# Optimization experiments

Measured on AMD Instinct MI355X. Metric: run time of the kernel, lower is better.

Reference implementation:

```python
import jax, jax.numpy as jnp
import numpy as np


def setup_inputs() -> dict:
    key = jax.random.key(0)
    ks = jax.random.split(key, 8)
    n_src, n_dst, n_edges = 100000, 50000, 600000
    d_in, d_out = 128, 128
    n_reuse, n_cache = 5000, 8000
    full_dst_len = n_dst + n_reuse

    feat_src = jax.random.normal(ks[0], (n_src, d_in), jnp.float32)
    src = jax.random.randint(ks[1], (n_edges,), 0, n_src)
    dst = jax.random.randint(ks[2], (n_edges,), 0, n_dst)
    # xavier-ish init for the two bias-free Linear layers (stored as [out, in] like torch)
    W_self = jax.random.normal(ks[3], (d_out, d_in), jnp.float32) / np.sqrt(d_in).astype(np.float32)
    W_neigh = jax.random.normal(ks[4], (d_out, d_in), jnp.float32) / np.sqrt(d_in).astype(np.float32)
    # reuse_indices must be unique positions within [0, full_dst_len)
    reuse_indices = jnp.sort(jax.random.permutation(ks[5], full_dst_len)[:n_reuse])
    reuse_embedding = jax.random.normal(ks[6], (n_reuse, d_out), jnp.float32)
    cache_indices = jax.random.randint(ks[7], (n_cache,), 0, full_dst_len)
    return dict(feat_src=feat_src, W_self=W_self, W_neigh=W_neigh,
                reuse_embedding=reuse_embedding, src=src, dst=dst,
                reuse_indices=reuse_indices, cache_indices=cache_indices,
                n_dst=n_dst)


def reference(feat_src, W_self, W_neigh, reuse_embedding, src, dst,
              reuse_indices, cache_indices, n_dst):
    # --- GraphSAGE 'mean' aggregation on a block graph ---
    feat_dst = feat_src[:n_dst]                         # [n_dst, D_in]
    msgs = feat_src[src]                                # [E, D_in] copy_src gather
    ssum = jax.ops.segment_sum(msgs, dst, num_segments=n_dst)          # [n_dst, D_in]
    deg = jax.ops.segment_sum(jnp.ones_like(msgs[:, 0]), dst, num_segments=n_dst)
    h_neigh = jnp.where(deg[:, None] > 0, ssum / jnp.maximum(deg, 1.0)[:, None], 0.0)
    rst = feat_dst @ W_self.T + h_neigh @ W_neigh.T     # fc_self + fc_neigh

    # --- cache-reuse scatter merge (flag == 0 path) ---
    n_reuse = reuse_indices.shape[0]
    full_dst_len = n_dst + n_reuse
    keep = jnp.ones((full_dst_len,), dtype=bool).at[reuse_indices].set(False)
    unprune_indices = jnp.nonzero(keep, size=n_dst)[0]  # np.delete equivalent
    full = jnp.zeros((full_dst_len, rst.shape[1]), rst.dtype)
    full = full.at[unprune_indices].set(rst).at[reuse_indices].set(reuse_embedding)
    cache_embedding = jax.lax.stop_gradient(full[cache_indices])  # .detach()
    return full, cache_embedding
```

## Files before the change

kernel.cpp:

```cpp
#include <hip/hip_runtime.h>

#define N_DST   50000
#define D       128
#define MAXDEG  128

typedef __attribute__((ext_vector_type(8))) short bf16x8;
typedef __attribute__((ext_vector_type(4))) float f32x4;

__device__ __forceinline__ unsigned short f2bf(float f) {
    unsigned u = __float_as_uint(f);
    u += 0x7FFFu + ((u >> 16) & 1u);
    return (unsigned short)(u >> 16);
}

__global__ void build_ell_kernel(const int* __restrict__ src,
                                 const int* __restrict__ dst,
                                 int* __restrict__ ell,
                                 int* __restrict__ cnt,
                                 int n_edges) {
    int e = blockIdx.x * blockDim.x + threadIdx.x;
    if (e >= n_edges) return;
    int d = dst[e];
    int pos = atomicAdd(&cnt[d], 1);
    if (pos < MAXDEG)
        ell[(size_t)d * MAXDEG + pos] = src[e];
}

__global__ void rowpos_kernel(const int* __restrict__ reuse_idx,
                              int* __restrict__ rowpos, int n_reuse) {
    int i = blockIdx.x * blockDim.x + threadIdx.x;
    if (i >= N_DST) return;
    int lo = 0, hi = n_reuse;
    while (lo < hi) {
        int mid = (lo + hi) >> 1;
        if (reuse_idx[mid] - mid > i) hi = mid; else lo = mid + 1;
    }
    rowpos[i] = i + lo;
}

__global__ void wconv_kernel(const float* __restrict__ Wself,
                             const float* __restrict__ Wneigh,
                             unsigned short* __restrict__ wbf) {
    int idx = blockIdx.x * blockDim.x + threadIdx.x;
    if (idx >= 128 * 256) return;
    int n = idx >> 8;
    int k = idx & 255;
    float v = (k < 128) ? Wself[n * 128 + k] : Wneigh[n * 128 + (k - 128)];
    wbf[idx] = f2bf(v);
}

__global__ __launch_bounds__(256)
void gather_kernel(const float* __restrict__ feat,
                   const int* __restrict__ ell,
                   const int* __restrict__ cnt,
                   unsigned int* __restrict__ hneigh_u32) {
    int gid  = blockIdx.x * blockDim.x + threadIdx.x;
    int row  = gid >> 6;
    int lane = threadIdx.x & 63;
    if (row >= N_DST) return;

    int deg = cnt[row];
    int n = min(deg, MAXDEG);
    float inv = 1.0f / fmaxf((float)deg, 1.0f);
    const int* rell = ell + (size_t)row * MAXDEG;

    float2 acc = make_float2(0.f, 0.f);
    int j = 0;
    for (; j + 4 <= n; j += 4) {
        int s0 = rell[j + 0];
        int s1 = rell[j + 1];
        int s2 = rell[j + 2];
        int s3 = rell[j + 3];
        float2 v0 = *(const float2*)&feat[(size_t)s0 * D + 2 * lane];
        float2 v1 = *(const float2*)&feat[(size_t)s1 * D + 2 * lane];
        float2 v2 = *(const float2*)&feat[(size_t)s2 * D + 2 * lane];
        float2 v3 = *(const float2*)&feat[(size_t)s3 * D + 2 * lane];
        acc.x += v0.x + v1.x + v2.x + v3.x;
        acc.y += v0.y + v1.y + v2.y + v3.y;
    }
    for (; j < n; ++j) {
        int s = rell[j];
        float2 v = *(const float2*)&feat[(size_t)s * D + 2 * lane];
        acc.x += v.x;
        acc.y += v.y;
    }
    unsigned lo16 = f2bf(acc.x * inv);
    unsigned hi16 = f2bf(acc.y * inv);
    hneigh_u32[(size_t)row * 64 + lane] = lo16 | (hi16 << 16);
}

__global__ __launch_bounds__(256, 2)
void gemm_kernel(const float* __restrict__ feat,
                 const unsigned short* __restrict__ hneigh,
                 const unsigned short* __restrict__ wbf,
                 const int* __restrict__ rowpos,
                 float* __restrict__ full) {
    __shared__ unsigned short Wl[128 * 256];

    int tid = threadIdx.x;
    {
        int n = tid >> 1;
        int ckbase = (tid & 1) * 16;
        const uint4* s = (const uint4*)(wbf + n * 256);
        uint4* d = (uint4*)(Wl + n * 256);
#pragma unroll
        for (int i = 0; i < 16; ++i) {
            int ck = ckbase + i;
            d[ck ^ (n & 7)] = s[ck];
        }
    }
    __syncthreads();

    int wv   = tid >> 6;
    int lane = tid & 63;
    int l15  = lane & 15;
    int q    = lane >> 4;
    int rowbase = blockIdx.x * 128 + wv * 32;

    f32x4 acc[2][8];
#pragma unroll
    for (int rt = 0; rt < 2; ++rt)
#pragma unroll
        for (int ct = 0; ct < 8; ++ct) acc[rt][ct] = (f32x4){0.f, 0.f, 0.f, 0.f};

    int r0c = min(rowbase + l15,      N_DST - 1);
    int r1c = min(rowbase + 16 + l15, N_DST - 1);

#pragma unroll 1
    for (int s = 0; s < 4; ++s) {
        int k0 = s * 32 + q * 8;
        float4 a0lo = *(const float4*)(feat + (size_t)r0c * D + k0);
        float4 a0hi = *(const float4*)(feat + (size_t)r0c * D + k0 + 4);
        float4 a1lo = *(const float4*)(feat + (size_t)r1c * D + k0);
        float4 a1hi = *(const float4*)(feat + (size_t)r1c * D + k0 + 4);
        union { bf16x8 v; unsigned short u[8]; } a0, a1;
        a0.u[0] = f2bf(a0lo.x); a0.u[1] = f2bf(a0lo.y);
        a0.u[2] = f2bf(a0lo.z); a0.u[3] = f2bf(a0lo.w);
        a0.u[4] = f2bf(a0hi.x); a0.u[5] = f2bf(a0hi.y);
        a0.u[6] = f2bf(a0hi.z); a0.u[7] = f2bf(a0hi.w);
        a1.u[0] = f2bf(a1lo.x); a1.u[1] = f2bf(a1lo.y);
        a1.u[2] = f2bf(a1lo.z); a1.u[3] = f2bf(a1lo.w);
        a1.u[4] = f2bf(a1hi.x); a1.u[5] = f2bf(a1hi.y);
        a1.u[6] = f2bf(a1hi.z); a1.u[7] = f2bf(a1hi.w);
#pragma unroll
        for (int ct = 0; ct < 8; ++ct) {
            int n = ct * 16 + l15;
            int ck = s * 4 + q;
            bf16x8 b = *(const bf16x8*)(Wl + n * 256 + ((ck ^ (n & 7)) << 3));
            acc[0][ct] = __builtin_amdgcn_mfma_f32_16x16x32_bf16(a0.v, b, acc[0][ct], 0, 0, 0);
            acc[1][ct] = __builtin_amdgcn_mfma_f32_16x16x32_bf16(a1.v, b, acc[1][ct], 0, 0, 0);
        }
    }
#pragma unroll 1
    for (int s = 0; s < 4; ++s) {
        int k0 = s * 32 + q * 8;
        bf16x8 a0 = *(const bf16x8*)(hneigh + (size_t)r0c * D + k0);
        bf16x8 a1 = *(const bf16x8*)(hneigh + (size_t)r1c * D + k0);
#pragma unroll
        for (int ct = 0; ct < 8; ++ct) {
            int n = ct * 16 + l15;
            int ck = 16 + s * 4 + q;
            bf16x8 b = *(const bf16x8*)(Wl + n * 256 + ((ck ^ (n & 7)) << 3));
            acc[0][ct] = __builtin_amdgcn_mfma_f32_16x16x32_bf16(a0, b, acc[0][ct], 0, 0, 0);
            acc[1][ct] = __builtin_amdgcn_mfma_f32_16x16x32_bf16(a1, b, acc[1][ct], 0, 0, 0);
        }
    }

#pragma unroll
    for (int rt = 0; rt < 2; ++rt) {
#pragma unroll
        for (int reg = 0; reg < 4; ++reg) {
            int gm = rowbase + rt * 16 + q * 4 + reg;
            if (gm < N_DST) {
                int jj = rowpos[gm];
                float* outr = full + (size_t)jj * D + l15;
#pragma unroll
                for (int ct = 0; ct < 8; ++ct)
                    outr[ct * 16] = acc[rt][ct][reg];
            }
        }
    }
}

__global__ void reuse_copy_kernel(const float* __restrict__ emb,
                                  const int* __restrict__ ridx,
                                  float* __restrict__ full, int n) {
    int idx = blockIdx.x * blockDim.x + threadIdx.x;
    int r = idx >> 5;
    if (r >= n) return;
    int c4 = (idx & 31) * 4;
    *(float4*)&full[ridx[r] * D + c4] = *(const float4*)&emb[r * D + c4];
}

__global__ void cache_gather_kernel(const float* __restrict__ full,
                                    const int* __restrict__ cidx,
                                    float* __restrict__ out, int n) {
    int idx = blockIdx.x * blockDim.x + threadIdx.x;
    int r = idx >> 5;
    if (r >= n) return;
    int c4 = (idx & 31) * 4;
    *(float4*)&out[r * D + c4] = *(const float4*)&full[cidx[r] * D + c4];
}

extern "C" void kernel_launch(void* const* d_in, const int* in_sizes, int n_in,
                              void* d_out, int out_size, void* d_ws, size_t ws_size,
                              hipStream_t stream) {
    const float* feat_src  = (const float*)d_in[0];
    const float* W_self    = (const float*)d_in[1];
    const float* W_neigh   = (const float*)d_in[2];
    const float* reuse_emb = (const float*)d_in[3];
    const int*   src       = (const int*)d_in[4];
    const int*   dst       = (const int*)d_in[5];
    const int*   reuse_idx = (const int*)d_in[6];
    const int*   cache_idx = (const int*)d_in[7];

    int n_edges = in_sizes[4];
    int n_reuse = in_sizes[6];
    int n_cache = in_sizes[7];
    int full_len = N_DST + n_reuse;

    unsigned short* hneigh = (unsigned short*)d_ws;
    int*   cnt    = (int*)(hneigh + (size_t)N_DST * D);
    int*   rowpos = cnt + N_DST;
    unsigned short* wbf = (unsigned short*)(rowpos + N_DST);

    float* full = (float*)d_out;
    float* cache_out = full + (size_t)full_len * D;

    int* ell = (int*)full;

    hipMemsetAsync(cnt, 0, (size_t)N_DST * sizeof(int), stream);

    build_ell_kernel<<<(n_edges + 255) / 256, 256, 0, stream>>>(
        src, dst, ell, cnt, n_edges);

    rowpos_kernel<<<(N_DST + 255) / 256, 256, 0, stream>>>(
        reuse_idx, rowpos, n_reuse);

    wconv_kernel<<<(128 * 256 + 255) / 256, 256, 0, stream>>>(
        W_self, W_neigh, wbf);

    gather_kernel<<<(N_DST * 64 + 255) / 256, 256, 0, stream>>>(
        feat_src, ell, cnt, (unsigned int*)hneigh);

    gemm_kernel<<<(N_DST + 127) / 128, 256, 0, stream>>>(
        feat_src, hneigh, wbf, rowpos, full);

    reuse_copy_kernel<<<(n_reuse * 32 + 255) / 256, 256, 0, stream>>>(
        reuse_emb, reuse_idx, full, n_reuse);

    cache_gather_kernel<<<(n_cache * 32 + 255) / 256, 256, 0, stream>>>(
        full, cache_idx, cache_out, n_cache);
}
```

Measured before the change: 204.9 us.

## Fuse neighbor gather with GEMM over a bf16 feature copy, merge prep kernels

```diff
diff --git a/kernel.cpp b/kernel.cpp
--- a/kernel.cpp
+++ b/kernel.cpp
@@ -2,7 +2,8 @@
 
 #define N_DST   50000
 #define D       128
-#define MAXDEG  128
+#define ELLW    64
+#define ELLW_FB 128
 
 typedef __attribute__((ext_vector_type(8))) short bf16x8;
 typedef __attribute__((ext_vector_type(4))) float f32x4;
@@ -12,65 +13,179 @@
     u += 0x7FFFu + ((u >> 16) & 1u);
     return (unsigned short)(u >> 16);
 }
+__device__ __forceinline__ void acc8_add(float* a, uint4 p) {
+    a[0] += __uint_as_float(p.x << 16);
+    a[1] += __uint_as_float(p.x & 0xffff0000u);
+    a[2] += __uint_as_float(p.y << 16);
+    a[3] += __uint_as_float(p.y & 0xffff0000u);
+    a[4] += __uint_as_float(p.z << 16);
+    a[5] += __uint_as_float(p.z & 0xffff0000u);
+    a[6] += __uint_as_float(p.w << 16);
+    a[7] += __uint_as_float(p.w & 0xffff0000u);
+}
 
 __global__ void build_ell_kernel(const int* __restrict__ src,
                                  const int* __restrict__ dst,
                                  int* __restrict__ ell,
                                  int* __restrict__ cnt,
-                                 int n_edges) {
+                                 int n_edges, int width) {
     int e = blockIdx.x * blockDim.x + threadIdx.x;
     if (e >= n_edges) return;
     int d = dst[e];
     int pos = atomicAdd(&cnt[d], 1);
-    if (pos < MAXDEG)
-        ell[(size_t)d * MAXDEG + pos] = src[e];
-}
-
-__global__ void rowpos_kernel(const int* __restrict__ reuse_idx,
-                              int* __restrict__ rowpos, int n_reuse) {
-    int i = blockIdx.x * blockDim.x + threadIdx.x;
-    if (i >= N_DST) return;
-    int lo = 0, hi = n_reuse;
-    while (lo < hi) {
-        int mid = (lo + hi) >> 1;
-        if (reuse_idx[mid] - mid > i) hi = mid; else lo = mid + 1;
-    }
-    rowpos[i] = i + lo;
-}
-
-__global__ void wconv_kernel(const float* __restrict__ Wself,
-                             const float* __restrict__ Wneigh,
-                             unsigned short* __restrict__ wbf) {
+    if (pos < width)
+        ell[(size_t)d * width + pos] = src[e];
+}
+
+__global__ void prep_kernel(const float* __restrict__ feat,
+                            const float* __restrict__ Wself,
+                            const float* __restrict__ Wneigh,
+                            const int* __restrict__ reuse_idx,
+                            unsigned short* __restrict__ featb,
+                            unsigned short* __restrict__ wbf,
+                            int* __restrict__ rowpos,
+                            int n_src16, int n_reuse) {
     int idx = blockIdx.x * blockDim.x + threadIdx.x;
-    if (idx >= 128 * 256) return;
-    int n = idx >> 8;
-    int k = idx & 255;
-    float v = (k < 128) ? Wself[n * 128 + k] : Wneigh[n * 128 + (k - 128)];
-    wbf[idx] = f2bf(v);
+    if (featb != nullptr && idx < n_src16) {
+        const float* s = feat + (size_t)idx * 8;
+        float4 v0 = *(const float4*)s;
+        float4 v1 = *(const float4*)(s + 4);
+        union { unsigned short u[8]; uint4 q; } o;
+        o.u[0] = f2bf(v0.x); o.u[1] = f2bf(v0.y);
+        o.u[2] = f2bf(v0.z); o.u[3] = f2bf(v0.w);
+        o.u[4] = f2bf(v1.x); o.u[5] = f2bf(v1.y);
+        o.u[6] = f2bf(v1.z); o.u[7] = f2bf(v1.w);
+        *(uint4*)(featb + (size_t)idx * 8) = o.q;
+    }
+    if (idx < 128 * 256) {
+        int n = idx >> 8, k = idx & 255;
+        float v = (k < 128) ? Wself[n * 128 + k] : Wneigh[n * 128 + (k - 128)];
+        wbf[idx] = f2bf(v);
+    }
+    if (idx < N_DST) {
+        int lo = 0, hi = n_reuse;
+        while (lo < hi) {
+            int m = (lo + hi) >> 1;
+            if (reuse_idx[m] - m > idx) hi = m; else lo = m + 1;
+        }
+        rowpos[idx] = idx + lo;
+    }
+}
+
+#define HNS 136
+__global__ __launch_bounds__(256, 4)
+void fused_kernel(const unsigned short* __restrict__ featb,
+                  const int* __restrict__ ell,
+                  const int* __restrict__ cnt,
+                  const unsigned short* __restrict__ wbf,
+                  const int* __restrict__ rowpos,
+                  float* __restrict__ full) {
+    __shared__ unsigned short hnl[64 * HNS];
+
+    int tid = threadIdx.x;
+    int r0 = blockIdx.x * 64;
+
+    {
+        int c = tid & 15;
+        int rowslot = tid >> 4;
+#pragma unroll 1
+        for (int i = 0; i < 4; ++i) {
+            int rl = rowslot + 16 * i;
+            int row = r0 + rl;
+            float acc[8] = {0.f, 0.f, 0.f, 0.f, 0.f, 0.f, 0.f, 0.f};
+            if (row < N_DST) {
+                int deg = cnt[row];
+                int n = min(deg, ELLW);
+                const int* rell = ell + (size_t)row * ELLW;
+                int j = 0;
+                for (; j + 4 <= n; j += 4) {
+                    int s0 = rell[j + 0];
+                    int s1 = rell[j + 1];
+                    int s2 = rell[j + 2];
+                    int s3 = rell[j + 3];
+                    uint4 p0 = *(const uint4*)(featb + (size_t)s0 * D + 8 * c);
+                    uint4 p1 = *(const uint4*)(featb + (size_t)s1 * D + 8 * c);
+                    uint4 p2 = *(const uint4*)(featb + (size_t)s2 * D + 8 * c);
+                    uint4 p3 = *(const uint4*)(featb + (size_t)s3 * D + 8 * c);
+                    acc8_add(acc, p0); acc8_add(acc, p1);
+                    acc8_add(acc, p2); acc8_add(acc, p3);
+                }
+                for (; j < n; ++j) {
+                    int s = rell[j];
+                    uint4 p = *(const uint4*)(featb + (size_t)s * D + 8 * c);
+                    acc8_add(acc, p);
+                }
+                float inv = 1.0f / fmaxf((float)deg, 1.0f);
+#pragma unroll
+                for (int k = 0; k < 8; ++k) acc[k] *= inv;
+            }
+            union { unsigned short u[8]; uint4 q; } o;
+#pragma unroll
+            for (int k = 0; k < 8; ++k) o.u[k] = f2bf(acc[k]);
+            *(uint4*)&hnl[rl * HNS + 8 * c] = o.q;
+        }
+    }
+    __syncthreads();
+
+    int wv = tid >> 6, lane = tid & 63;
+    int l15 = lane & 15, q = lane >> 4;
+    int rowbase = r0 + wv * 16;
+
+    f32x4 acc[8];
+#pragma unroll
+    for (int ct = 0; ct < 8; ++ct) acc[ct] = (f32x4){0.f, 0.f, 0.f, 0.f};
+
+    int rA = min(rowbase + l15, N_DST - 1);
+    const unsigned short* aptr = featb + (size_t)rA * D;
+#pragma unroll 1
+    for (int s = 0; s < 4; ++s) {
+        bf16x8 a = *(const bf16x8*)(aptr + s * 32 + q * 8);
+#pragma unroll
+        for (int ct = 0; ct < 8; ++ct) {
+            bf16x8 b = *(const bf16x8*)(wbf + (ct * 16 + l15) * 256 + s * 32 + q * 8);
+            acc[ct] = __builtin_amdgcn_mfma_f32_16x16x32_bf16(a, b, acc[ct], 0, 0, 0);
+        }
+    }
+    const unsigned short* hrow = hnl + (wv * 16 + l15) * HNS;
+#pragma unroll 1
+    for (int s = 0; s < 4; ++s) {
+        bf16x8 a = *(const bf16x8*)(hrow + s * 32 + q * 8);
+#pragma unroll
+        for (int ct = 0; ct < 8; ++ct) {
+            bf16x8 b = *(const bf16x8*)(wbf + (ct * 16 + l15) * 256 + 128 + s * 32 + q * 8);
+            acc[ct] = __builtin_amdgcn_mfma_f32_16x16x32_bf16(a, b, acc[ct], 0, 0, 0);
+        }
+    }
+
+#pragma unroll
+    for (int reg = 0; reg < 4; ++reg) {
+        int gm = rowbase + q * 4 + reg;
+        if (gm < N_DST) {
+            float* outr = full + (size_t)rowpos[gm] * D + l15;
+#pragma unroll
+            for (int ct = 0; ct < 8; ++ct)
+                outr[ct * 16] = acc[ct][reg];
+        }
+    }
 }
 
 __global__ __launch_bounds__(256)
-void gather_kernel(const float* __restrict__ feat,
-                   const int* __restrict__ ell,
-                   const int* __restrict__ cnt,
-                   unsigned int* __restrict__ hneigh_u32) {
+void gather_fb_kernel(const float* __restrict__ feat,
+                      const int* __restrict__ ell,
+                      const int* __restrict__ cnt,
+                      unsigned int* __restrict__ hneigh_u32) {
     int gid  = blockIdx.x * blockDim.x + threadIdx.x;
     int row  = gid >> 6;
     int lane = threadIdx.x & 63;
     if (row >= N_DST) return;
-
     int deg = cnt[row];
-    int n = min(deg, MAXDEG);
+    int n = min(deg, ELLW_FB);
     float inv = 1.0f / fmaxf((float)deg, 1.0f);
-    const int* rell = ell + (size_t)row * MAXDEG;
-
+    const int* rell = ell + (size_t)row * ELLW_FB;
     float2 acc = make_float2(0.f, 0.f);
     int j = 0;
     for (; j + 4 <= n; j += 4) {
-        int s0 = rell[j + 0];
-        int s1 = rell[j + 1];
-        int s2 = rell[j + 2];
-        int s3 = rell[j + 3];
+        int s0 = rell[j + 0], s1 = rell[j + 1], s2 = rell[j + 2], s3 = rell[j + 3];
         float2 v0 = *(const float2*)&feat[(size_t)s0 * D + 2 * lane];
         float2 v1 = *(const float2*)&feat[(size_t)s1 * D + 2 * lane];
         float2 v2 = *(const float2*)&feat[(size_t)s2 * D + 2 * lane];
@@ -81,8 +196,7 @@
     for (; j < n; ++j) {
         int s = rell[j];
         float2 v = *(const float2*)&feat[(size_t)s * D + 2 * lane];
-        acc.x += v.x;
-        acc.y += v.y;
+        acc.x += v.x; acc.y += v.y;
     }
     unsigned lo16 = f2bf(acc.x * inv);
     unsigned hi16 = f2bf(acc.y * inv);
@@ -90,13 +204,12 @@
 }
 
 __global__ __launch_bounds__(256, 2)
-void gemm_kernel(const float* __restrict__ feat,
-                 const unsigned short* __restrict__ hneigh,
-                 const unsigned short* __restrict__ wbf,
-                 const int* __restrict__ rowpos,
-                 float* __restrict__ full) {
+void gemm_fb_kernel(const float* __restrict__ feat,
+                    const unsigned short* __restrict__ hneigh,
+                    const unsigned short* __restrict__ wbf,
+                    const int* __restrict__ rowpos,
+                    float* __restrict__ full) {
     __shared__ unsigned short Wl[128 * 256];
-
     int tid = threadIdx.x;
     {
         int n = tid >> 1;
@@ -110,22 +223,15 @@
         }
     }
     __syncthreads();
-
-    int wv   = tid >> 6;
-    int lane = tid & 63;
-    int l15  = lane & 15;
-    int q    = lane >> 4;
+    int wv = tid >> 6, lane = tid & 63, l15 = lane & 15, q = lane >> 4;
     int rowbase = blockIdx.x * 128 + wv * 32;
-
     f32x4 acc[2][8];
 #pragma unroll
     for (int rt = 0; rt < 2; ++rt)
 #pragma unroll
         for (int ct = 0; ct < 8; ++ct) acc[rt][ct] = (f32x4){0.f, 0.f, 0.f, 0.f};
-
     int r0c = min(rowbase + l15,      N_DST - 1);
     int r1c = min(rowbase + 16 + l15, N_DST - 1);
-
 #pragma unroll 1
     for (int s = 0; s < 4; ++s) {
         int k0 = s * 32 + q * 8;
@@ -165,15 +271,13 @@
             acc[1][ct] = __builtin_amdgcn_mfma_f32_16x16x32_bf16(a1, b, acc[1][ct], 0, 0, 0);
         }
     }
-
 #pragma unroll
     for (int rt = 0; rt < 2; ++rt) {
 #pragma unroll
         for (int reg = 0; reg < 4; ++reg) {
             int gm = rowbase + rt * 16 + q * 4 + reg;
             if (gm < N_DST) {
-                int jj = rowpos[gm];
-                float* outr = full + (size_t)jj * D + l15;
+                float* outr = full + (size_t)rowpos[gm] * D + l15;
 #pragma unroll
                 for (int ct = 0; ct < 8; ++ct)
                     outr[ct * 16] = acc[rt][ct][reg];
@@ -182,24 +286,32 @@
     }
 }
 
-__global__ void reuse_copy_kernel(const float* __restrict__ emb,
-                                  const int* __restrict__ ridx,
-                                  float* __restrict__ full, int n) {
+__global__ void finalize_kernel(const float* __restrict__ emb,
+                                const int* __restrict__ ridx,
+                                const int* __restrict__ cidx,
+                                float* __restrict__ full,
+                                float* __restrict__ cache_out,
+                                int n_reuse, int n_cache) {
     int idx = blockIdx.x * blockDim.x + threadIdx.x;
     int r = idx >> 5;
-    if (r >= n) return;
     int c4 = (idx & 31) * 4;
-    *(float4*)&full[ridx[r] * D + c4] = *(const float4*)&emb[r * D + c4];
-}
-
-__global__ void cache_gather_kernel(const float* __restrict__ full,
-                                    const int* __restrict__ cidx,
-                                    float* __restrict__ out, int n) {
-    int idx = blockIdx.x * blockDim.x + threadIdx.x;
-    int r = idx >> 5;
-    if (r >= n) return;
-    int c4 = (idx & 31) * 4;
-    *(float4*)&out[r * D + c4] = *(const float4*)&full[cidx[r] * D + c4];
+    if (r < n_reuse) {
+        *(float4*)&full[(size_t)ridx[r] * D + c4] = *(const float4*)&emb[(size_t)r * D + c4];
+    } else if (r < n_reuse + n_cache) {
+        int t = r - n_reuse;
+        int j = cidx[t];
+        int lo = 0, hi = n_reuse;
+        while (lo < hi) {
+            int m = (lo + hi) >> 1;
+            if (ridx[m] < j) lo = m + 1; else hi = m;
+        }
+        float4 v;
+        if (lo < n_reuse && ridx[lo] == j)
+            v = *(const float4*)&emb[(size_t)lo * D + c4];
+        else
+            v = *(const float4*)&full[(size_t)j * D + c4];
+        *(float4*)&cache_out[(size_t)t * D + c4] = v;
+    }
 }
 
 extern "C" void kernel_launch(void* const* d_in, const int* in_sizes, int n_in,
@@ -214,41 +326,57 @@
     const int*   reuse_idx = (const int*)d_in[6];
     const int*   cache_idx = (const int*)d_in[7];
 
+    int n_src   = in_sizes[0] / D;
     int n_edges = in_sizes[4];
     int n_reuse = in_sizes[6];
     int n_cache = in_sizes[7];
     int full_len = N_DST + n_reuse;
 
-    unsigned short* hneigh = (unsigned short*)d_ws;
-    int*   cnt    = (int*)(hneigh + (size_t)N_DST * D);
-    int*   rowpos = cnt + N_DST;
-    unsigned short* wbf = (unsigned short*)(rowpos + N_DST);
-
     float* full = (float*)d_out;
     float* cache_out = full + (size_t)full_len * D;
 
-    int* ell = (int*)full;
+    int* cnt    = (int*)cache_out;
+    int* rowpos = cnt + N_DST;
+    unsigned short* wbf = (unsigned short*)(rowpos + N_DST);
 
     hipMemsetAsync(cnt, 0, (size_t)N_DST * sizeof(int), stream);
 
-    build_ell_kernel<<<(n_edges + 255) / 256, 256, 0, stream>>>(
-        src, dst, ell, cnt, n_edges);
-
-    rowpos_kernel<<<(N_DST + 255) / 256, 256, 0, stream>>>(
-        reuse_idx, rowpos, n_reuse);
-
-    wconv_kernel<<<(128 * 256 + 255) / 256, 256, 0, stream>>>(
-        W_self, W_neigh, wbf);
-
-    gather_kernel<<<(N_DST * 64 + 255) / 256, 256, 0, stream>>>(
-        feat_src, ell, cnt, (unsigned int*)hneigh);
-
-    gemm_kernel<<<(N_DST + 127) / 128, 256, 0, stream>>>(
-        feat_src, hneigh, wbf, rowpos, full);
-
-    reuse_copy_kernel<<<(n_reuse * 32 + 255) / 256, 256, 0, stream>>>(
-        reuse_emb, reuse_idx, full, n_reuse);
-
-    cache_gather_kernel<<<(n_cache * 32 + 255) / 256, 256, 0, stream>>>(
-        full, cache_idx, cache_out, n_cache);
-}
+    size_t featb_bytes = (size_t)n_src * D * sizeof(unsigned short);
+    size_t ell_bytes   = (size_t)N_DST * ELLW * sizeof(int);
+
+    if (ws_size >= featb_bytes + ell_bytes) {
+        unsigned short* featb = (unsigned short*)d_ws;
+        int* ell = (int*)((char*)d_ws + featb_bytes);
+
+        build_ell_kernel<<<(n_edges + 255) / 256, 256, 0, stream>>>(
+            src, dst, ell, cnt, n_edges, ELLW);
+
+        int n_src16 = n_src * 16;
+        prep_kernel<<<(n_src16 + 255) / 256, 256, 0, stream>>>(
+            feat_src, W_self, W_neigh, reuse_idx, featb, wbf, rowpos,
+            n_src16, n_reuse);
+
+        fused_kernel<<<(N_DST + 63) / 64, 256, 0, stream>>>(
+            featb, ell, cnt, wbf, rowpos, full);
+    } else {
+        int* ell = (int*)full;
+        unsigned short* hneigh = (unsigned short*)d_ws;
+
+        build_ell_kernel<<<(n_edges + 255) / 256, 256, 0, stream>>>(
+            src, dst, ell, cnt, n_edges, ELLW_FB);
+
+        prep_kernel<<<(N_DST + 255) / 256, 256, 0, stream>>>(
+            feat_src, W_self, W_neigh, reuse_idx, nullptr, wbf, rowpos,
+            0, n_reuse);
+
+        gather_fb_kernel<<<(N_DST * 64 + 255) / 256, 256, 0, stream>>>(
+            feat_src, ell, cnt, (unsigned int*)hneigh);
+
+        gemm_fb_kernel<<<(N_DST + 127) / 128, 256, 0, stream>>>(
+            feat_src, hneigh, wbf, rowpos, full);
+    }
+
+    int fin_rows = n_reuse + n_cache;
+    finalize_kernel<<<(fin_rows * 32 + 255) / 256, 256, 0, stream>>>(
+        reuse_emb, reuse_idx, cache_idx, full, cache_out, n_reuse, n_cache);
+}
```

Result: no change. 206.4 us (+0.7%).
